# Optimization experiments

Measured on AMD Instinct MI355X. Metric: run time of the kernel, lower is better.

## Reference

```python
import jax, jax.numpy as jnp
import numpy as np

B, N, M, D, OUT, K = 8, 32, 64, 128, 128, 3
EPS = 1e-5


def batchnorm(x, g, b):
    # training-mode BatchNorm2d over NCHW (stats over B,H,W per channel, biased var)
    mean = x.mean((0, 2, 3), keepdims=True)
    var = ((x - mean) ** 2).mean((0, 2, 3), keepdims=True)
    return g[None, :, None, None] * (x - mean) * jax.lax.rsqrt(var + EPS) + b[None, :, None, None]


def mycorr(x):
    # Pearson correlation between nodes along feature dim: x (B,M,N,D) -> (B,M,N,N)
    xc = x - x.mean(-1, keepdims=True)
    num = jnp.einsum('bmid,bmjd->bmij', xc, xc)
    nrm = jnp.sqrt((xc * xc).sum(-1))
    return num / (nrm[:, :, :, None] * nrm[:, :, None, :] + 1e-8)


def attention(x, W_fc1, W_fc2):
    # x: (B,M,N,D). AdaptiveAvgPool2d((None,1)) over the concat [Wh_i, pos*Wh_j]
    # equals 0.5*(mean_d Wh_i + mean_d(pos*Wh_j)); pos=1 where Wh_i==Wh_j else 2.
    adj = mycorr(x)
    mean_i = x.mean(-1)                       # (B,M,N)
    xi = x[:, :, :, None, :]                  # (B,M,N,1,D)
    xj = x[:, :, None, :, :]                  # (B,M,1,N,D)
    alt_mean = jnp.where(xi == xj, xj, 2.0 * xj).mean(-1)  # (B,M,N,N)
    e = 0.5 * (mean_i[:, :, :, None] + alt_mean)            # (B,M,N,N)
    ef = e.reshape(e.shape[0], e.shape[1], -1)              # (B,M,N*N) pair channels
    h = jax.nn.relu(jnp.einsum('rp,bmp->bmr', W_fc1, ef))
    e2 = jax.nn.sigmoid(jnp.einsum('pr,bmr->bmp', W_fc2, h)).reshape(e.shape)
    att = jax.nn.softmax(jnp.where(adj > 0, e2, jnp.float32(-1e12)), axis=-1)
    return jnp.einsum('bmij,bmjd->bmid', att, x)


def setup_inputs() -> dict:
    key = jax.random.key(0)
    ks = jax.random.split(key, 8)
    P, r, s = N * N, (N * N) // 2, 0.05
    return {
        'x': jax.random.normal(ks[0], (B, N, M, D), jnp.float32),
        'W_sc': jax.random.normal(ks[1], (OUT, M), jnp.float32) * s,
        'g_sc': jnp.ones(OUT, jnp.float32), 'b_sc': jnp.zeros(OUT, jnp.float32),
        'W_l1': jax.random.normal(ks[2], (M, M), jnp.float32) * s,
        'g1': jnp.ones(M, jnp.float32), 'b1': jnp.zeros(M, jnp.float32),
        'W_fc1': jax.random.normal(ks[3], (r, P), jnp.float32) * s,
        'W_fc2': jax.random.normal(ks[4], (P, r), jnp.float32) * s,
        'g2': jnp.ones(M, jnp.float32), 'b2': jnp.zeros(M, jnp.float32),
        'W_dw': jax.random.normal(ks[5], (N, 1, K, K), jnp.float32) * s,
        'g3': jnp.ones(N, jnp.float32), 'b3': jnp.zeros(N, jnp.float32),
        'W_l3': jax.random.normal(ks[6], (OUT, M), jnp.float32) * s,
    }


def reference(x, W_sc, g_sc, b_sc, W_l1, g1, b1, W_fc1, W_fc2, g2, b2, W_dw, g3, b3, W_l3):
    xm = jnp.transpose(x, (0, 2, 1, 3))  # (B,M,N,D)
    # shortcut: 1x1 conv over head channel + BN (stride=1 path)
    shortcut = batchnorm(jnp.einsum('om,bmnd->bond', W_sc, xm), g_sc, b_sc)
    # layer_1: 1x1 conv, BN, global node attention, BN, ReLU
    out = batchnorm(jnp.einsum('cm,bmnd->bcnd', W_l1, xm), g1, b1)
    out = attention(out, W_fc1, W_fc2)
    out = jax.nn.relu(batchnorm(out, g2, b2))
    # layer_2: depthwise KxK conv over (head, dim) per node, BN, ReLU
    out = jnp.transpose(out, (0, 2, 1, 3))  # (B,N,M,D)
    pad = K // 2
    out = jax.lax.conv_general_dilated(out, W_dw, (1, 1), ((pad, pad), (pad, pad)),
                                       feature_group_count=N,
                                       dimension_numbers=('NCHW', 'OIHW', 'NCHW'))
    out = jax.nn.relu(batchnorm(out, g3, b3))
    # layer_3: 1x1 conv to out_channels heads + residual
    out = jnp.transpose(out, (0, 2, 1, 3))  # (B,M,N,D)
    out = jnp.einsum('om,bmnd->bond', W_l3, out) + shortcut
    return jnp.transpose(out, (0, 2, 1, 3))  # (B,N,OUT,D)
```

## Files before the change

kernel.cpp:

```cpp
#include <hip/hip_runtime.h>
#include <math.h>

#define EPS 1e-5f


__device__ __forceinline__ void fma4(float4& a, float s, const float4& v) {
    a.x += s * v.x; a.y += s * v.y; a.z += s * v.z; a.w += s * v.w;
}

__global__ __launch_bounds__(256) void k1_matmul_stats(
    const float* __restrict__ x, const float* __restrict__ Wsc,
    const float* __restrict__ Wl1, float* __restrict__ t_sc,
    float* __restrict__ t_l1, float* __restrict__ stats)
{
    int g  = blockIdx.x;
    int bn = blockIdx.y;
    int b = bn >> 5, n = bn & 31;
    __shared__ __align__(16) float s_x[64 * 128];
    __shared__ __align__(16) float s_wT[64 * 68];
    int t = threadIdx.x;

    const float4* xg = (const float4*)(x + (size_t)bn * 8192);
    for (int i = t; i < 2048; i += 256) ((float4*)s_x)[i] = xg[i];

    const float* wbase = (g < 2) ? (Wsc + (size_t)g * 64 * 64) : Wl1;
    for (int i = t; i < 1024; i += 256) {
        int m = i >> 4, rq = (i & 15) * 4;
        float4 wv;
        wv.x = wbase[(size_t)(rq + 0) * 64 + m];
        wv.y = wbase[(size_t)(rq + 1) * 64 + m];
        wv.z = wbase[(size_t)(rq + 2) * 64 + m];
        wv.w = wbase[(size_t)(rq + 3) * 64 + m];
        *(float4*)(s_wT + m * 68 + rq) = wv;
    }
    __syncthreads();

    int wv = t >> 6, lane = t & 63;
    int dl = lane & 15;
    int g4 = lane >> 4;
    int d0 = dl * 8;
    int c0 = wv * 16 + g4 * 4;

    float4 acc[4][2];
#pragma unroll
    for (int i = 0; i < 4; i++) { acc[i][0] = make_float4(0,0,0,0); acc[i][1] = make_float4(0,0,0,0); }

    for (int m = 0; m < 64; m += 2) {
        float4 x00 = *(const float4*)(s_x + m * 128 + d0);
        float4 x01 = *(const float4*)(s_x + m * 128 + d0 + 4);
        float4 x10 = *(const float4*)(s_x + (m + 1) * 128 + d0);
        float4 x11 = *(const float4*)(s_x + (m + 1) * 128 + d0 + 4);
        float4 w0 = *(const float4*)(s_wT + m * 68 + c0);
        float4 w1 = *(const float4*)(s_wT + (m + 1) * 68 + c0);
        fma4(acc[0][0], w0.x, x00); fma4(acc[0][1], w0.x, x01);
        fma4(acc[1][0], w0.y, x00); fma4(acc[1][1], w0.y, x01);
        fma4(acc[2][0], w0.z, x00); fma4(acc[2][1], w0.z, x01);
        fma4(acc[3][0], w0.w, x00); fma4(acc[3][1], w0.w, x01);
        fma4(acc[0][0], w1.x, x10); fma4(acc[0][1], w1.x, x11);
        fma4(acc[1][0], w1.y, x10); fma4(acc[1][1], w1.y, x11);
        fma4(acc[2][0], w1.z, x10); fma4(acc[2][1], w1.z, x11);
        fma4(acc[3][0], w1.w, x10); fma4(acc[3][1], w1.w, x11);
    }

#pragma unroll
    for (int i = 0; i < 4; i++) {
        int cc = g * 64 + c0 + i;
        float4 v0 = acc[i][0], v1 = acc[i][1];
        float* dst;
        if (cc < 128) dst = t_sc + (((size_t)(b * 128 + cc)) * 32 + n) * 128 + d0;
        else          dst = t_l1 + (((size_t)(b * 64 + (cc - 128))) * 32 + n) * 128 + d0;
        *(float4*)dst = v0;
        *(float4*)(dst + 4) = v1;
        float s = v0.x + v0.y + v0.z + v0.w + v1.x + v1.y + v1.z + v1.w;
        float q = v0.x*v0.x + v0.y*v0.y + v0.z*v0.z + v0.w*v0.w
                + v1.x*v1.x + v1.y*v1.y + v1.z*v1.z + v1.w*v1.w;
#pragma unroll
        for (int off = 8; off > 0; off >>= 1) {
            s += __shfl_down(s, off, 16);
            q += __shfl_down(q, off, 16);
        }
        if (dl == 0) {
            if (cc < 128) {
                atomicAdd(&stats[cc], s);
                atomicAdd(&stats[cc + 128], q);
            } else {
                atomicAdd(&stats[256 + (cc - 128)], s);
                atomicAdd(&stats[320 + (cc - 128)], q);
            }
        }
    }
}

__global__ __launch_bounds__(256) void k2_attn_prep(
    const float* __restrict__ t_l1, const float* __restrict__ g1,
    const float* __restrict__ b1, const float* __restrict__ stats,
    float* __restrict__ y_g, float* __restrict__ E,
    unsigned int* __restrict__ maskbits)
{
    int bm = blockIdx.x;
    int t  = threadIdx.x;
    __shared__ __align__(16) float y_s[32 * 132];
    __shared__ float S_s[32];
    __shared__ unsigned int m_s[32];
    int m = bm & 63;
    float mean = stats[256 + m] * (1.0f / 32768.0f);
    float var  = stats[320 + m] * (1.0f / 32768.0f) - mean * mean;
    float a = g1[m] * rsqrtf(var + EPS);
    float c = b1[m] - a * mean;

    if (t < 32) m_s[t] = 0u;
    const float4* src = (const float4*)(t_l1 + (size_t)bm * 4096);
    for (int i = t; i < 1024; i += 256) {
        float4 v = src[i];
        v.x = a * v.x + c; v.y = a * v.y + c; v.z = a * v.z + c; v.w = a * v.w + c;
        int row = i >> 5, col = (i & 31) * 4;
        *(float4*)(y_s + row * 132 + col) = v;
    }
    __syncthreads();

    {
        int r = t >> 3, j = t & 7;
        float s = 0.f;
        const float* yr = y_s + r * 132 + j * 16;
#pragma unroll
        for (int dd = 0; dd < 16; dd++) s += yr[dd];
#pragma unroll
        for (int off = 4; off > 0; off >>= 1) s += __shfl_down(s, off, 8);
        if (j == 0) S_s[r] = s;
    }
    __syncthreads();

    int i = t >> 3, j0 = (t & 7) * 4;
    float dot[4] = {0.f, 0.f, 0.f, 0.f};
    float eqs[4] = {0.f, 0.f, 0.f, 0.f};
    const float* yi = y_s + i * 132;
    for (int dq = 0; dq < 32; dq++) {
        float4 a4 = *(const float4*)(yi + dq * 4);
#pragma unroll
        for (int q = 0; q < 4; q++) {
            float4 b4 = *(const float4*)(y_s + (j0 + q) * 132 + dq * 4);
            dot[q] += a4.x * b4.x + a4.y * b4.y + a4.z * b4.z + a4.w * b4.w;
            eqs[q] += (a4.x == b4.x ? b4.x : 0.f) + (a4.y == b4.y ? b4.y : 0.f)
                    + (a4.z == b4.z ? b4.z : 0.f) + (a4.w == b4.w ? b4.w : 0.f);
        }
    }
    float Si = S_s[i];
    unsigned int bits = 0u;
    float ev[4];
#pragma unroll
    for (int q = 0; q < 4; q++) {
        float Sj = S_s[j0 + q];
        float num = dot[q] - Si * Sj * (1.0f / 128.0f);
        if (num > 0.f) bits |= (1u << (j0 + q));
        ev[q] = (Si + 2.f * Sj - eqs[q]) * (1.0f / 256.0f);
    }
    atomicOr(&m_s[i], bits);
    *(float4*)(E + (size_t)bm * 1024 + i * 32 + j0) = make_float4(ev[0], ev[1], ev[2], ev[3]);
    __syncthreads();
    if (t < 32) maskbits[bm * 32 + t] = m_s[t];

    float4* yd = (float4*)(y_g + (size_t)bm * 4096);
    for (int idx = t; idx < 1024; idx += 256) {
        int row = idx >> 5, col = (idx & 31) * 4;
        yd[idx] = *(const float4*)(y_s + row * 132 + col);
    }
}

template<int KDIM, int MODE>
__global__ __launch_bounds__(256) void k3_gemm(
    const float* __restrict__ A, const float* __restrict__ Bm,
    float* __restrict__ C, int NC)
{
    __shared__ __align__(16) float lds[4 * 2304];
    int t = threadIdx.x;
    int w = t >> 6, l = t & 63;
    int ct = blockIdx.x, rt = blockIdx.y;
    int row0 = rt * 32, col0 = ct * 32;
    float* As = lds + w * 2304;
    float* Bs = As + 1152;
    int rg = l >> 3;
    int cg = l & 7;
    int kq = (l & 7) * 4;
    constexpr int SLABS = KDIM / 128;

    float4 acc[4];
#pragma unroll
    for (int ii = 0; ii < 4; ii++) acc[ii] = make_float4(0,0,0,0);

    float4 av[4], bv[4], av2[4], bv2[4];
    int k0 = w * 32;
#pragma unroll
    for (int rr = 0; rr < 4; rr++) {
        int r = rg + rr * 8;
        av[rr] = *(const float4*)(A  + (size_t)(row0 + r) * KDIM + k0 + kq);
        bv[rr] = *(const float4*)(Bm + (size_t)(col0 + r) * KDIM + k0 + kq);
    }

    for (int s = 0; s < SLABS; s++) {
#pragma unroll
        for (int rr = 0; rr < 4; rr++) {
            int r = rg + rr * 8;
            As[(kq + 0) * 36 + r] = av[rr].x; As[(kq + 1) * 36 + r] = av[rr].y;
            As[(kq + 2) * 36 + r] = av[rr].z; As[(kq + 3) * 36 + r] = av[rr].w;
            Bs[(kq + 0) * 36 + r] = bv[rr].x; Bs[(kq + 1) * 36 + r] = bv[rr].y;
            Bs[(kq + 2) * 36 + r] = bv[rr].z; Bs[(kq + 3) * 36 + r] = bv[rr].w;
        }
        if (s + 1 < SLABS) {
            int kn = (4 * (s + 1) + w) * 32;
#pragma unroll
            for (int rr = 0; rr < 4; rr++) {
                int r = rg + rr * 8;
                av2[rr] = *(const float4*)(A  + (size_t)(row0 + r) * KDIM + kn + kq);
                bv2[rr] = *(const float4*)(Bm + (size_t)(col0 + r) * KDIM + kn + kq);
            }
        }
#pragma unroll
        for (int k = 0; k < 32; k++) {
            float4 a = *(const float4*)(As + k * 36 + rg * 4);
            float4 b = *(const float4*)(Bs + k * 36 + cg * 4);
            fma4(acc[0], a.x, b);
            fma4(acc[1], a.y, b);
            fma4(acc[2], a.z, b);
            fma4(acc[3], a.w, b);
        }
#pragma unroll
        for (int rr = 0; rr < 4; rr++) { av[rr] = av2[rr]; bv[rr] = bv2[rr]; }
    }

    __syncthreads();
    float* red = lds;
#pragma unroll
    for (int ii = 0; ii < 4; ii++)
        *(float4*)(red + w * 1024 + (rg * 4 + ii) * 32 + cg * 4) = acc[ii];
    __syncthreads();

    int r = t >> 3, c4 = (t & 7) * 4;
    float4 s0 = *(const float4*)(red + r * 32 + c4);
    float4 s1 = *(const float4*)(red + 1024 + r * 32 + c4);
    float4 s2 = *(const float4*)(red + 2048 + r * 32 + c4);
    float4 s3 = *(const float4*)(red + 3072 + r * 32 + c4);
    float4 v;
    v.x = s0.x + s1.x + s2.x + s3.x;
    v.y = s0.y + s1.y + s2.y + s3.y;
    v.z = s0.z + s1.z + s2.z + s3.z;
    v.w = s0.w + s1.w + s2.w + s3.w;
    if (MODE == 0) {
        v.x = fmaxf(v.x, 0.f); v.y = fmaxf(v.y, 0.f);
        v.z = fmaxf(v.z, 0.f); v.w = fmaxf(v.w, 0.f);
    } else {
        v.x = 1.0f / (1.0f + expf(-v.x)); v.y = 1.0f / (1.0f + expf(-v.y));
        v.z = 1.0f / (1.0f + expf(-v.z)); v.w = 1.0f / (1.0f + expf(-v.w));
    }
    *(float4*)(C + (size_t)(row0 + r) * NC + col0 + c4) = v;
}

__global__ __launch_bounds__(256) void k4_attn_apply(
    const float* __restrict__ E2, const unsigned int* __restrict__ maskbits,
    const float* __restrict__ y_g, float* __restrict__ att_out,
    float* __restrict__ stats)
{
    int bm = blockIdx.x;
    int t  = threadIdx.x;
    __shared__ __align__(16) float att_s[32 * 33];
    __shared__ __align__(16) float y_sh[32 * 128];
    __shared__ float redS[4], redQ[4];

    const float4* ysrc = (const float4*)(y_g + (size_t)bm * 4096);
    float4* yds = (float4*)y_sh;
    for (int i = t; i < 1024; i += 256) yds[i] = ysrc[i];

    {
        int r = t >> 3, j0 = (t & 7) * 4;
        unsigned int mk = maskbits[bm * 32 + r];
        float4 e4 = *(const float4*)(E2 + (size_t)bm * 1024 + r * 32 + j0);
        float v0 = ((mk >> (j0 + 0)) & 1u) ? e4.x : -1e12f;
        float v1 = ((mk >> (j0 + 1)) & 1u) ? e4.y : -1e12f;
        float v2 = ((mk >> (j0 + 2)) & 1u) ? e4.z : -1e12f;
        float v3 = ((mk >> (j0 + 3)) & 1u) ? e4.w : -1e12f;
        float mx = fmaxf(fmaxf(v0, v1), fmaxf(v2, v3));
#pragma unroll
        for (int off = 1; off < 8; off <<= 1) mx = fmaxf(mx, __shfl_xor(mx, off, 8));
        float e0 = __expf(v0 - mx), e1 = __expf(v1 - mx);
        float e2 = __expf(v2 - mx), e3 = __expf(v3 - mx);
        float s = e0 + e1 + e2 + e3;
#pragma unroll
        for (int off = 1; off < 8; off <<= 1) s += __shfl_xor(s, off, 8);
        float inv = 1.0f / s;
        att_s[r * 33 + j0 + 0] = e0 * inv;
        att_s[r * 33 + j0 + 1] = e1 * inv;
        att_s[r * 33 + j0 + 2] = e2 * inv;
        att_s[r * 33 + j0 + 3] = e3 * inv;
    }
    __syncthreads();

    int tx = t & 31, ty = t >> 5;
    int dq = tx * 4;
    float ssum = 0.f, sq = 0.f;
#pragma unroll
    for (int ii = 0; ii < 4; ii++) {
        int i = ty * 4 + ii;
        float4 acc = make_float4(0.f, 0.f, 0.f, 0.f);
        for (int j = 0; j < 32; j++) {
            float aw = att_s[i * 33 + j];
            float4 yv = *(const float4*)(y_sh + j * 128 + dq);
            acc.x += aw * yv.x; acc.y += aw * yv.y;
            acc.z += aw * yv.z; acc.w += aw * yv.w;
        }
        *(float4*)(att_out + (size_t)bm * 4096 + i * 128 + dq) = acc;
        ssum += acc.x + acc.y + acc.z + acc.w;
        sq   += acc.x * acc.x + acc.y * acc.y + acc.z * acc.z + acc.w * acc.w;
    }
#pragma unroll
    for (int off = 32; off > 0; off >>= 1) {
        ssum += __shfl_down(ssum, off, 64);
        sq   += __shfl_down(sq, off, 64);
    }
    int wave = t >> 6, lane = t & 63;
    if (lane == 0) { redS[wave] = ssum; redQ[wave] = sq; }
    __syncthreads();
    if (t == 0) {
        float S = redS[0] + redS[1] + redS[2] + redS[3];
        float Q = redQ[0] + redQ[1] + redQ[2] + redQ[3];
        int m = bm & 63;
        atomicAdd(&stats[384 + m], S);
        atomicAdd(&stats[448 + m], Q);
    }
}

__global__ __launch_bounds__(256) void k5_conv(
    const float* __restrict__ att_out, const float* __restrict__ Wdw,
    const float* __restrict__ g2, const float* __restrict__ b2,
    float* __restrict__ stats, float* __restrict__ v_g)
{
    int bn = blockIdx.x;
    int b = bn >> 5, n = bn & 31;
    int t = threadIdx.x;
    __shared__ __align__(16) float z_s[66 * 130];
    __shared__ float a2_s[64], c2_s[64];
    __shared__ float redS[4], redQ[4];

    if (t < 64) {
        float mean = stats[384 + t] * (1.0f / 32768.0f);
        float var  = stats[448 + t] * (1.0f / 32768.0f) - mean * mean;
        float a = g2[t] * rsqrtf(var + EPS);
        a2_s[t] = a; c2_s[t] = b2[t] - a * mean;
    }
    for (int i = t; i < 66 * 130; i += 256) z_s[i] = 0.f;
    __syncthreads();

    for (int i = t; i < 2048; i += 256) {
        int m = i >> 5, c4 = (i & 31) * 4;
        float4 vv = *(const float4*)(att_out + (((size_t)(b * 64 + m)) * 32 + n) * 128 + c4);
        float a = a2_s[m], c = c2_s[m];
        float* dst = z_s + (m + 1) * 130 + c4 + 1;
        dst[0] = fmaxf(a * vv.x + c, 0.f);
        dst[1] = fmaxf(a * vv.y + c, 0.f);
        dst[2] = fmaxf(a * vv.z + c, 0.f);
        dst[3] = fmaxf(a * vv.w + c, 0.f);
    }
    float w[9];
#pragma unroll
    for (int i = 0; i < 9; i++) w[i] = Wdw[n * 9 + i];
    __syncthreads();

    int tx = t & 31, ty = t >> 5;
    int d0 = tx * 4;
    float ssum = 0.f, sq = 0.f;
#pragma unroll
    for (int rr = 0; rr < 8; rr++) {
        int h = ty * 8 + rr;
        float o0 = 0.f, o1 = 0.f, o2 = 0.f, o3 = 0.f;
#pragma unroll
        for (int dh = 0; dh < 3; dh++) {
            const float* zr = z_s + (h + dh) * 130 + d0;
#pragma unroll
            for (int dw = 0; dw < 3; dw++) {
                float wv = w[dh * 3 + dw];
                o0 += wv * zr[dw + 0];
                o1 += wv * zr[dw + 1];
                o2 += wv * zr[dw + 2];
                o3 += wv * zr[dw + 3];
            }
        }
        *(float4*)(v_g + ((size_t)bn * 64 + h) * 128 + d0) = make_float4(o0, o1, o2, o3);
        ssum += o0 + o1 + o2 + o3;
        sq   += o0 * o0 + o1 * o1 + o2 * o2 + o3 * o3;
    }
#pragma unroll
    for (int off = 32; off > 0; off >>= 1) {
        ssum += __shfl_down(ssum, off, 64);
        sq   += __shfl_down(sq, off, 64);
    }
    int wave = t >> 6, lane = t & 63;
    if (lane == 0) { redS[wave] = ssum; redQ[wave] = sq; }
    __syncthreads();
    if (t == 0) {
        atomicAdd(&stats[512 + n], redS[0] + redS[1] + redS[2] + redS[3]);
        atomicAdd(&stats[544 + n], redQ[0] + redQ[1] + redQ[2] + redQ[3]);
    }
}

__global__ __launch_bounds__(256) void k6_final(
    const float* __restrict__ v_g, const float* __restrict__ t_sc,
    const float* __restrict__ Wl3, const float* __restrict__ g3,
    const float* __restrict__ b3, const float* __restrict__ gsc,
    const float* __restrict__ bsc, const float* __restrict__ stats,
    float* __restrict__ outp)
{
    int oh = blockIdx.x;
    int bn = blockIdx.y;
    int b = bn >> 5, n = bn & 31;
    int t = threadIdx.x;
    __shared__ __align__(16) float z_s[64 * 128];
    __shared__ __align__(16) float s_wT[64 * 68];

    float mean3 = stats[512 + n] * (1.0f / 65536.0f);
    float var3  = stats[544 + n] * (1.0f / 65536.0f) - mean3 * mean3;
    float a3 = g3[n] * rsqrtf(var3 + EPS);
    float c3 = b3[n] - a3 * mean3;

    const float4* vsrc = (const float4*)(v_g + (size_t)bn * 8192);
    for (int i = t; i < 2048; i += 256) {
        float4 vv = vsrc[i];
        float4 r;
        r.x = fmaxf(a3 * vv.x + c3, 0.f);
        r.y = fmaxf(a3 * vv.y + c3, 0.f);
        r.z = fmaxf(a3 * vv.z + c3, 0.f);
        r.w = fmaxf(a3 * vv.w + c3, 0.f);
        ((float4*)z_s)[i] = r;
    }
    const float* wbase = Wl3 + (size_t)oh * 64 * 64;
    for (int i = t; i < 1024; i += 256) {
        int m = i >> 4, rq = (i & 15) * 4;
        float4 wv;
        wv.x = wbase[(size_t)(rq + 0) * 64 + m];
        wv.y = wbase[(size_t)(rq + 1) * 64 + m];
        wv.z = wbase[(size_t)(rq + 2) * 64 + m];
        wv.w = wbase[(size_t)(rq + 3) * 64 + m];
        *(float4*)(s_wT + m * 68 + rq) = wv;
    }
    __syncthreads();

    int wv = t >> 6, lane = t & 63;
    int dl = lane & 15, g4 = lane >> 4;
    int d0 = dl * 8;
    int c0 = wv * 16 + g4 * 4;

    float4 acc[4][2];
#pragma unroll
    for (int i = 0; i < 4; i++) { acc[i][0] = make_float4(0,0,0,0); acc[i][1] = make_float4(0,0,0,0); }

    for (int m = 0; m < 64; m += 2) {
        float4 x00 = *(const float4*)(z_s + m * 128 + d0);
        float4 x01 = *(const float4*)(z_s + m * 128 + d0 + 4);
        float4 x10 = *(const float4*)(z_s + (m + 1) * 128 + d0);
        float4 x11 = *(const float4*)(z_s + (m + 1) * 128 + d0 + 4);
        float4 w0 = *(const float4*)(s_wT + m * 68 + c0);
        float4 w1 = *(const float4*)(s_wT + (m + 1) * 68 + c0);
        fma4(acc[0][0], w0.x, x00); fma4(acc[0][1], w0.x, x01);
        fma4(acc[1][0], w0.y, x00); fma4(acc[1][1], w0.y, x01);
        fma4(acc[2][0], w0.z, x00); fma4(acc[2][1], w0.z, x01);
        fma4(acc[3][0], w0.w, x00); fma4(acc[3][1], w0.w, x01);
        fma4(acc[0][0], w1.x, x10); fma4(acc[0][1], w1.x, x11);
        fma4(acc[1][0], w1.y, x10); fma4(acc[1][1], w1.y, x11);
        fma4(acc[2][0], w1.z, x10); fma4(acc[2][1], w1.z, x11);
        fma4(acc[3][0], w1.w, x10); fma4(acc[3][1], w1.w, x11);
    }

#pragma unroll
    for (int i = 0; i < 4; i++) {
        int o = oh * 64 + c0 + i;
        float msc = stats[o] * (1.0f / 32768.0f);
        float vsc = stats[128 + o] * (1.0f / 32768.0f) - msc * msc;
        float asc = gsc[o] * rsqrtf(vsc + EPS);
        float csc = bsc[o] - asc * msc;
        const float* ts = t_sc + (((size_t)(b * 128 + o)) * 32 + n) * 128 + d0;
        float4 t0 = *(const float4*)(ts);
        float4 t1 = *(const float4*)(ts + 4);
        float4 o0 = acc[i][0], o1 = acc[i][1];
        o0.x += asc * t0.x + csc; o0.y += asc * t0.y + csc;
        o0.z += asc * t0.z + csc; o0.w += asc * t0.w + csc;
        o1.x += asc * t1.x + csc; o1.y += asc * t1.y + csc;
        o1.z += asc * t1.z + csc; o1.w += asc * t1.w + csc;
        float* dst = outp + (((size_t)(b * 32 + n)) * 128 + o) * 128 + d0;
        *(float4*)dst = o0;
        *(float4*)(dst + 4) = o1;
    }
}

extern "C" void kernel_launch(void* const* d_in, const int* in_sizes, int n_in,
                              void* d_out, int out_size, void* d_ws, size_t ws_size,
                              hipStream_t stream)
{
    const float* x    = (const float*)d_in[0];
    const float* Wsc  = (const float*)d_in[1];
    const float* gsc  = (const float*)d_in[2];
    const float* bsc  = (const float*)d_in[3];
    const float* Wl1  = (const float*)d_in[4];
    const float* g1   = (const float*)d_in[5];
    const float* b1   = (const float*)d_in[6];
    const float* Wfc1 = (const float*)d_in[7];
    const float* Wfc2 = (const float*)d_in[8];
    const float* g2   = (const float*)d_in[9];
    const float* b2   = (const float*)d_in[10];
    const float* Wdw  = (const float*)d_in[11];
    const float* g3   = (const float*)d_in[12];
    const float* b3   = (const float*)d_in[13];
    const float* Wl3  = (const float*)d_in[14];
    float* outp = (float*)d_out;

    float* ws = (float*)d_ws;
    float* stats = ws;
    float* t_sc  = ws + 1024;
    float* t_l1  = t_sc + 4194304;
    float* y_g   = t_l1 + 2097152;
    float* E     = y_g + 2097152;
    float* H     = E + 524288;
    float* E2    = H + 262144;
    unsigned int* maskb = (unsigned int*)(E2 + 524288);

    (void)hipMemsetAsync(stats, 0, 1024 * sizeof(float), stream);

    k1_matmul_stats<<<dim3(3, 256), 256, 0, stream>>>(x, Wsc, Wl1, t_sc, t_l1, stats);
    k2_attn_prep<<<512, 256, 0, stream>>>(t_l1, g1, b1, stats, y_g, E, maskb);
    k3_gemm<1024, 0><<<dim3(16, 16), 256, 0, stream>>>(E, Wfc1, H, 512);
    k3_gemm<512, 1><<<dim3(32, 16), 256, 0, stream>>>(H, Wfc2, E2, 1024);
    k4_attn_apply<<<512, 256, 0, stream>>>(E2, maskb, y_g, t_l1, stats);
    k5_conv<<<256, 256, 0, stream>>>(t_l1, Wdw, g2, b2, stats, y_g);
    k6_final<<<dim3(2, 256), 256, 0, stream>>>(y_g, t_sc, Wl3, g3, b3, gsc, bsc, stats, outp);
}
```

Measured before the change: 210.5 us.

## Fuse all stages into one persistent cooperative kernel with grid syncs

Turns the seven stage kernels into device functions that share one union of shared memory, and runs them from a single persistent cooperative kernel. Stages are separated by grid-wide barriers, and each block loops over work units. The aim is to remove launch overhead and the gaps between kernels. In exchange, every block reserves the largest shared-memory footprint, the grid is capped at 256 or 512 blocks so each stage runs in fewer waves, and grid.sync adds cost; the separate-launch path remains as a fallback if the cooperative launch fails.

```diff
diff --git a/kernel.cpp b/kernel.cpp
--- a/kernel.cpp
+++ b/kernel.cpp
@@ -1,5 +1,8 @@
 #include <hip/hip_runtime.h>
+#include <hip/hip_cooperative_groups.h>
 #include <math.h>
+
+namespace cg = cooperative_groups;
 
 #define EPS 1e-5f
 
@@ -8,17 +11,23 @@
     a.x += s * v.x; a.y += s * v.y; a.z += s * v.z; a.w += s * v.w;
 }
 
-__global__ __launch_bounds__(256) void k1_matmul_stats(
-    const float* __restrict__ x, const float* __restrict__ Wsc,
+union SharedU {
+    struct { float s_x[64 * 128]; float s_wT[64 * 68]; } p1;
+    struct { float y_s[32 * 132]; float S_s[32]; unsigned int m_s[32]; } p2;
+    struct { float lds[4 * 2304]; } p3;
+    struct { float att_s[32 * 33]; float y_sh[32 * 128]; float redS[4], redQ[4]; } p5;
+    struct { float z_s[66 * 130]; float a2_s[64], c2_s[64]; float redS[4], redQ[4]; } p6;
+    struct { float z_s[64 * 128]; float s_wT[64 * 68]; } p7;
+};
+
+__device__ __forceinline__ void phase1(
+    SharedU& su, const float* __restrict__ x, const float* __restrict__ Wsc,
     const float* __restrict__ Wl1, float* __restrict__ t_sc,
-    float* __restrict__ t_l1, float* __restrict__ stats)
-{
-    int g  = blockIdx.x;
-    int bn = blockIdx.y;
+    float* __restrict__ t_l1, float* __restrict__ stats, int g, int bn, int t)
+{
+    float* s_x  = su.p1.s_x;
+    float* s_wT = su.p1.s_wT;
     int b = bn >> 5, n = bn & 31;
-    __shared__ __align__(16) float s_x[64 * 128];
-    __shared__ __align__(16) float s_wT[64 * 68];
-    int t = threadIdx.x;
 
     const float4* xg = (const float4*)(x + (size_t)bn * 8192);
     for (int i = t; i < 2048; i += 256) ((float4*)s_x)[i] = xg[i];
@@ -91,17 +100,15 @@
     }
 }
 
-__global__ __launch_bounds__(256) void k2_attn_prep(
-    const float* __restrict__ t_l1, const float* __restrict__ g1,
+__device__ __forceinline__ void phase2(
+    SharedU& su, const float* __restrict__ t_l1, const float* __restrict__ g1,
     const float* __restrict__ b1, const float* __restrict__ stats,
     float* __restrict__ y_g, float* __restrict__ E,
-    unsigned int* __restrict__ maskbits)
-{
-    int bm = blockIdx.x;
-    int t  = threadIdx.x;
-    __shared__ __align__(16) float y_s[32 * 132];
-    __shared__ float S_s[32];
-    __shared__ unsigned int m_s[32];
+    unsigned int* __restrict__ maskbits, int bm, int t)
+{
+    float* y_s = su.p2.y_s;
+    float* S_s = su.p2.S_s;
+    unsigned int* m_s = su.p2.m_s;
     int m = bm & 63;
     float mean = stats[256 + m] * (1.0f / 32768.0f);
     float var  = stats[320 + m] * (1.0f / 32768.0f) - mean * mean;
@@ -167,14 +174,12 @@
 }
 
 template<int KDIM, int MODE>
-__global__ __launch_bounds__(256) void k3_gemm(
-    const float* __restrict__ A, const float* __restrict__ Bm,
-    float* __restrict__ C, int NC)
-{
-    __shared__ __align__(16) float lds[4 * 2304];
-    int t = threadIdx.x;
+__device__ __forceinline__ void gemm_phase(
+    SharedU& su, const float* __restrict__ A, const float* __restrict__ Bm,
+    float* __restrict__ C, int NC, int ct, int rt, int t)
+{
+    float* lds = su.p3.lds;
     int w = t >> 6, l = t & 63;
-    int ct = blockIdx.x, rt = blockIdx.y;
     int row0 = rt * 32, col0 = ct * 32;
     float* As = lds + w * 2304;
     float* Bs = As + 1152;
@@ -254,16 +259,15 @@
     *(float4*)(C + (size_t)(row0 + r) * NC + col0 + c4) = v;
 }
 
-__global__ __launch_bounds__(256) void k4_attn_apply(
-    const float* __restrict__ E2, const unsigned int* __restrict__ maskbits,
-    const float* __restrict__ y_g, float* __restrict__ att_out,
-    float* __restrict__ stats)
-{
-    int bm = blockIdx.x;
-    int t  = threadIdx.x;
-    __shared__ __align__(16) float att_s[32 * 33];
-    __shared__ __align__(16) float y_sh[32 * 128];
-    __shared__ float redS[4], redQ[4];
+__device__ __forceinline__ void phase5(
+    SharedU& su, const float* __restrict__ E2,
+    const unsigned int* __restrict__ maskbits, const float* __restrict__ y_g,
+    float* __restrict__ att_out, float* __restrict__ stats, int bm, int t)
+{
+    float* att_s = su.p5.att_s;
+    float* y_sh  = su.p5.y_sh;
+    float* redS  = su.p5.redS;
+    float* redQ  = su.p5.redQ;
 
     const float4* ysrc = (const float4*)(y_g + (size_t)bm * 4096);
     float4* yds = (float4*)y_sh;
@@ -327,17 +331,17 @@
     }
 }
 
-__global__ __launch_bounds__(256) void k5_conv(
-    const float* __restrict__ att_out, const float* __restrict__ Wdw,
+__device__ __forceinline__ void phase6(
+    SharedU& su, const float* __restrict__ att_out, const float* __restrict__ Wdw,
     const float* __restrict__ g2, const float* __restrict__ b2,
-    float* __restrict__ stats, float* __restrict__ v_g)
-{
-    int bn = blockIdx.x;
+    float* __restrict__ stats, float* __restrict__ v_g, int bn, int t)
+{
+    float* z_s = su.p6.z_s;
+    float* a2_s = su.p6.a2_s;
+    float* c2_s = su.p6.c2_s;
+    float* redS = su.p6.redS;
+    float* redQ = su.p6.redQ;
     int b = bn >> 5, n = bn & 31;
-    int t = threadIdx.x;
-    __shared__ __align__(16) float z_s[66 * 130];
-    __shared__ float a2_s[64], c2_s[64];
-    __shared__ float redS[4], redQ[4];
 
     if (t < 64) {
         float mean = stats[384 + t] * (1.0f / 32768.0f);
@@ -400,19 +404,16 @@
     }
 }
 
-__global__ __launch_bounds__(256) void k6_final(
-    const float* __restrict__ v_g, const float* __restrict__ t_sc,
+__device__ __forceinline__ void phase7(
+    SharedU& su, const float* __restrict__ v_g, const float* __restrict__ t_sc,
     const float* __restrict__ Wl3, const float* __restrict__ g3,
     const float* __restrict__ b3, const float* __restrict__ gsc,
     const float* __restrict__ bsc, const float* __restrict__ stats,
-    float* __restrict__ outp)
-{
-    int oh = blockIdx.x;
-    int bn = blockIdx.y;
+    float* __restrict__ outp, int oh, int bn, int t)
+{
+    float* z_s  = su.p7.z_s;
+    float* s_wT = su.p7.s_wT;
     int b = bn >> 5, n = bn & 31;
-    int t = threadIdx.x;
-    __shared__ __align__(16) float z_s[64 * 128];
-    __shared__ __align__(16) float s_wT[64 * 68];
 
     float mean3 = stats[512 + n] * (1.0f / 65536.0f);
     float var3  = stats[544 + n] * (1.0f / 65536.0f) - mean3 * mean3;
@@ -488,6 +489,115 @@
     }
 }
 
+__global__ __launch_bounds__(256, 2) void mega(
+    const float* x, const float* Wsc, const float* gsc, const float* bsc,
+    const float* Wl1, const float* g1, const float* b1,
+    const float* Wfc1, const float* Wfc2, const float* g2, const float* b2,
+    const float* Wdw, const float* g3, const float* b3, const float* Wl3,
+    float* stats, float* t_sc, float* t_l1, float* y_g,
+    float* E, float* H, float* E2, unsigned int* maskb, float* outp)
+{
+    __shared__ SharedU su;
+    cg::grid_group grid = cg::this_grid();
+    int blk = blockIdx.x;
+    int t = threadIdx.x;
+    int gsz = gridDim.x;
+
+    for (int u = blk; u < 768; u += gsz) {
+        phase1(su, x, Wsc, Wl1, t_sc, t_l1, stats, u >> 8, u & 255, t);
+        __syncthreads();
+    }
+    grid.sync();
+
+    for (int u = blk; u < 512; u += gsz) {
+        phase2(su, t_l1, g1, b1, stats, y_g, E, maskb, u, t);
+        __syncthreads();
+    }
+    grid.sync();
+
+    for (int u = blk; u < 256; u += gsz) {
+        gemm_phase<1024, 0>(su, E, Wfc1, H, 512, u & 15, u >> 4, t);
+        __syncthreads();
+    }
+    grid.sync();
+
+    for (int u = blk; u < 512; u += gsz) {
+        gemm_phase<512, 1>(su, H, Wfc2, E2, 1024, u & 31, u >> 5, t);
+        __syncthreads();
+    }
+    grid.sync();
+
+    for (int u = blk; u < 512; u += gsz) {
+        phase5(su, E2, maskb, y_g, t_l1, stats, u, t);
+        __syncthreads();
+    }
+    grid.sync();
+
+    for (int u = blk; u < 256; u += gsz) {
+        phase6(su, t_l1, Wdw, g2, b2, stats, y_g, u, t);
+        __syncthreads();
+    }
+    grid.sync();
+
+    for (int u = blk; u < 512; u += gsz) {
+        phase7(su, y_g, t_sc, Wl3, g3, b3, gsc, bsc, stats, outp, u & 1, u >> 1, t);
+        __syncthreads();
+    }
+}
+
+__global__ __launch_bounds__(256) void k1_w(
+    const float* __restrict__ x, const float* __restrict__ Wsc,
+    const float* __restrict__ Wl1, float* __restrict__ t_sc,
+    float* __restrict__ t_l1, float* __restrict__ stats)
+{
+    __shared__ SharedU su;
+    phase1(su, x, Wsc, Wl1, t_sc, t_l1, stats, blockIdx.x, blockIdx.y, threadIdx.x);
+}
+__global__ __launch_bounds__(256) void k2_w(
+    const float* __restrict__ t_l1, const float* __restrict__ g1,
+    const float* __restrict__ b1, const float* __restrict__ stats,
+    float* __restrict__ y_g, float* __restrict__ E,
+    unsigned int* __restrict__ maskbits)
+{
+    __shared__ SharedU su;
+    phase2(su, t_l1, g1, b1, stats, y_g, E, maskbits, blockIdx.x, threadIdx.x);
+}
+template<int KDIM, int MODE>
+__global__ __launch_bounds__(256) void k3_w(
+    const float* __restrict__ A, const float* __restrict__ Bm,
+    float* __restrict__ C, int NC)
+{
+    __shared__ SharedU su;
+    gemm_phase<KDIM, MODE>(su, A, Bm, C, NC, blockIdx.x, blockIdx.y, threadIdx.x);
+}
+__global__ __launch_bounds__(256) void k5_w(
+    const float* __restrict__ E2, const unsigned int* __restrict__ maskbits,
+    const float* __restrict__ y_g, float* __restrict__ att_out,
+    float* __restrict__ stats)
+{
+    __shared__ SharedU su;
+    phase5(su, E2, maskbits, y_g, att_out, stats, blockIdx.x, threadIdx.x);
+}
+__global__ __launch_bounds__(256) void k6_w(
+    const float* __restrict__ att_out, const float* __restrict__ Wdw,
+    const float* __restrict__ g2, const float* __restrict__ b2,
+    float* __restrict__ stats, float* __restrict__ v_g)
+{
+    __shared__ SharedU su;
+    phase6(su, att_out, Wdw, g2, b2, stats, v_g, blockIdx.x, threadIdx.x);
+}
+__global__ __launch_bounds__(256) void k7_w(
+    const float* __restrict__ v_g, const float* __restrict__ t_sc,
+    const float* __restrict__ Wl3, const float* __restrict__ g3,
+    const float* __restrict__ b3, const float* __restrict__ gsc,
+    const float* __restrict__ bsc, const float* __restrict__ stats,
+    float* __restrict__ outp)
+{
+    __shared__ SharedU su;
+    phase7(su, v_g, t_sc, Wl3, g3, b3, gsc, bsc, stats, outp,
+           blockIdx.x, blockIdx.y, threadIdx.x);
+}
+
 extern "C" void kernel_launch(void* const* d_in, const int* in_sizes, int n_in,
                               void* d_out, int out_size, void* d_ws, size_t ws_size,
                               hipStream_t stream)
@@ -521,11 +631,26 @@
 
     (void)hipMemsetAsync(stats, 0, 1024 * sizeof(float), stream);
 
-    k1_matmul_stats<<<dim3(3, 256), 256, 0, stream>>>(x, Wsc, Wl1, t_sc, t_l1, stats);
-    k2_attn_prep<<<512, 256, 0, stream>>>(t_l1, g1, b1, stats, y_g, E, maskb);
-    k3_gemm<1024, 0><<<dim3(16, 16), 256, 0, stream>>>(E, Wfc1, H, 512);
-    k3_gemm<512, 1><<<dim3(32, 16), 256, 0, stream>>>(H, Wfc2, E2, 1024);
-    k4_attn_apply<<<512, 256, 0, stream>>>(E2, maskb, y_g, t_l1, stats);
-    k5_conv<<<256, 256, 0, stream>>>(t_l1, Wdw, g2, b2, stats, y_g);
-    k6_final<<<dim3(2, 256), 256, 0, stream>>>(y_g, t_sc, Wl3, g3, b3, gsc, bsc, stats, outp);
-}
+    int perCU = 0;
+    hipError_t qerr = hipOccupancyMaxActiveBlocksPerMultiprocessor(&perCU, mega, 256, 0);
+    int nblk = (qerr == hipSuccess && perCU >= 2) ? 512 : 256;
+
+    void* args[] = {
+        (void*)&x, (void*)&Wsc, (void*)&gsc, (void*)&bsc, (void*)&Wl1,
+        (void*)&g1, (void*)&b1, (void*)&Wfc1, (void*)&Wfc2, (void*)&g2,
+        (void*)&b2, (void*)&Wdw, (void*)&g3, (void*)&b3, (void*)&Wl3,
+        (void*)&stats, (void*)&t_sc, (void*)&t_l1, (void*)&y_g,
+        (void*)&E, (void*)&H, (void*)&E2, (void*)&maskb, (void*)&outp
+    };
+    hipError_t lerr = hipLaunchCooperativeKernel((void*)mega, dim3(nblk), dim3(256),
+                                                 args, 0, stream);
+    if (lerr != hipSuccess) {
+        k1_w<<<dim3(3, 256), 256, 0, stream>>>(x, Wsc, Wl1, t_sc, t_l1, stats);
+        k2_w<<<512, 256, 0, stream>>>(t_l1, g1, b1, stats, y_g, E, maskb);
+        k3_w<1024, 0><<<dim3(16, 16), 256, 0, stream>>>(E, Wfc1, H, 512);
+        k3_w<512, 1><<<dim3(32, 16), 256, 0, stream>>>(H, Wfc2, E2, 1024);
+        k5_w<<<512, 256, 0, stream>>>(E2, maskb, y_g, t_l1, stats);
+        k6_w<<<256, 256, 0, stream>>>(t_l1, Wdw, g2, b2, stats, y_g);
+        k7_w<<<dim3(2, 256), 256, 0, stream>>>(y_g, t_sc, Wl3, g3, b3, gsc, bsc, stats, outp);
+    }
+}
```

New measurement: 443.9 us. 111% more time.

## Split-K the attention FC GEMMs and double grid sizes of attention/conv kernels

Applied to the files above, without the earlier changes.

The two FC GEMMs now use split-K with two partial outputs, and the following kernels sum the partials and apply ReLU or sigmoid. This replaces the templated GEMM with activation epilogues. The attention-prep, attention-apply and depthwise conv kernels are each split in half (row halves or D halves, with halo loading for the conv), doubling block counts so more CUs stay busy. The cost is extra partial-buffer traffic and some redundant loads of shared inputs per half-block.

```diff
diff --git a/kernel.cpp b/kernel.cpp
--- a/kernel.cpp
+++ b/kernel.cpp
@@ -8,7 +8,7 @@
     a.x += s * v.x; a.y += s * v.y; a.z += s * v.z; a.w += s * v.w;
 }
 
-__global__ __launch_bounds__(256) void k1_matmul_stats(
+__global__ __launch_bounds__(256) void k1_w(
     const float* __restrict__ x, const float* __restrict__ Wsc,
     const float* __restrict__ Wl1, float* __restrict__ t_sc,
     float* __restrict__ t_l1, float* __restrict__ stats)
@@ -36,8 +36,7 @@
     __syncthreads();
 
     int wv = t >> 6, lane = t & 63;
-    int dl = lane & 15;
-    int g4 = lane >> 4;
+    int dl = lane & 15, g4 = lane >> 4;
     int d0 = dl * 8;
     int c0 = wv * 16 + g4 * 4;
 
@@ -91,30 +90,30 @@
     }
 }
 
-__global__ __launch_bounds__(256) void k2_attn_prep(
+__global__ __launch_bounds__(256) void k2_w(
     const float* __restrict__ t_l1, const float* __restrict__ g1,
     const float* __restrict__ b1, const float* __restrict__ stats,
     float* __restrict__ y_g, float* __restrict__ E,
     unsigned int* __restrict__ maskbits)
 {
-    int bm = blockIdx.x;
+    int blk = blockIdx.x;
+    int bm = blk >> 1, h = blk & 1;
     int t  = threadIdx.x;
     __shared__ __align__(16) float y_s[32 * 132];
     __shared__ float S_s[32];
-    __shared__ unsigned int m_s[32];
+    __shared__ unsigned int m_s[16];
     int m = bm & 63;
     float mean = stats[256 + m] * (1.0f / 32768.0f);
     float var  = stats[320 + m] * (1.0f / 32768.0f) - mean * mean;
     float a = g1[m] * rsqrtf(var + EPS);
     float c = b1[m] - a * mean;
 
-    if (t < 32) m_s[t] = 0u;
+    if (t < 16) m_s[t] = 0u;
     const float4* src = (const float4*)(t_l1 + (size_t)bm * 4096);
     for (int i = t; i < 1024; i += 256) {
         float4 v = src[i];
         v.x = a * v.x + c; v.y = a * v.y + c; v.z = a * v.z + c; v.w = a * v.w + c;
-        int row = i >> 5, col = (i & 31) * 4;
-        *(float4*)(y_s + row * 132 + col) = v;
+        *(float4*)(y_s + (i >> 5) * 132 + (i & 31) * 4) = v;
     }
     __syncthreads();
 
@@ -130,58 +129,61 @@
     }
     __syncthreads();
 
-    int i = t >> 3, j0 = (t & 7) * 4;
-    float dot[4] = {0.f, 0.f, 0.f, 0.f};
-    float eqs[4] = {0.f, 0.f, 0.f, 0.f};
-    const float* yi = y_s + i * 132;
+    int i_loc = t >> 4;
+    int i = h * 16 + i_loc;
+    int j0 = (t & 15) * 2;
+    float dot0 = 0.f, dot1 = 0.f, eq0 = 0.f, eq1 = 0.f;
+    const float* yi  = y_s + i * 132;
+    const float* yj0 = y_s + j0 * 132;
+    const float* yj1 = y_s + (j0 + 1) * 132;
     for (int dq = 0; dq < 32; dq++) {
         float4 a4 = *(const float4*)(yi + dq * 4);
-#pragma unroll
-        for (int q = 0; q < 4; q++) {
-            float4 b4 = *(const float4*)(y_s + (j0 + q) * 132 + dq * 4);
-            dot[q] += a4.x * b4.x + a4.y * b4.y + a4.z * b4.z + a4.w * b4.w;
-            eqs[q] += (a4.x == b4.x ? b4.x : 0.f) + (a4.y == b4.y ? b4.y : 0.f)
-                    + (a4.z == b4.z ? b4.z : 0.f) + (a4.w == b4.w ? b4.w : 0.f);
-        }
+        float4 b0 = *(const float4*)(yj0 + dq * 4);
+        float4 b1v = *(const float4*)(yj1 + dq * 4);
+        dot0 += a4.x * b0.x + a4.y * b0.y + a4.z * b0.z + a4.w * b0.w;
+        eq0  += (a4.x == b0.x ? b0.x : 0.f) + (a4.y == b0.y ? b0.y : 0.f)
+              + (a4.z == b0.z ? b0.z : 0.f) + (a4.w == b0.w ? b0.w : 0.f);
+        dot1 += a4.x * b1v.x + a4.y * b1v.y + a4.z * b1v.z + a4.w * b1v.w;
+        eq1  += (a4.x == b1v.x ? b1v.x : 0.f) + (a4.y == b1v.y ? b1v.y : 0.f)
+              + (a4.z == b1v.z ? b1v.z : 0.f) + (a4.w == b1v.w ? b1v.w : 0.f);
     }
     float Si = S_s[i];
+    float Sj0 = S_s[j0], Sj1 = S_s[j0 + 1];
     unsigned int bits = 0u;
-    float ev[4];
-#pragma unroll
-    for (int q = 0; q < 4; q++) {
-        float Sj = S_s[j0 + q];
-        float num = dot[q] - Si * Sj * (1.0f / 128.0f);
-        if (num > 0.f) bits |= (1u << (j0 + q));
-        ev[q] = (Si + 2.f * Sj - eqs[q]) * (1.0f / 256.0f);
-    }
-    atomicOr(&m_s[i], bits);
-    *(float4*)(E + (size_t)bm * 1024 + i * 32 + j0) = make_float4(ev[0], ev[1], ev[2], ev[3]);
-    __syncthreads();
-    if (t < 32) maskbits[bm * 32 + t] = m_s[t];
+    if (dot0 - Si * Sj0 * (1.0f / 128.0f) > 0.f) bits |= (1u << j0);
+    if (dot1 - Si * Sj1 * (1.0f / 128.0f) > 0.f) bits |= (1u << (j0 + 1));
+    float ev0 = (Si + 2.f * Sj0 - eq0) * (1.0f / 256.0f);
+    float ev1 = (Si + 2.f * Sj1 - eq1) * (1.0f / 256.0f);
+    atomicOr(&m_s[i_loc], bits);
+    *(float2*)(E + (size_t)bm * 1024 + i * 32 + j0) = make_float2(ev0, ev1);
+    __syncthreads();
+    if (t < 16) maskbits[bm * 32 + h * 16 + t] = m_s[t];
 
     float4* yd = (float4*)(y_g + (size_t)bm * 4096);
-    for (int idx = t; idx < 1024; idx += 256) {
-        int row = idx >> 5, col = (idx & 31) * 4;
-        yd[idx] = *(const float4*)(y_s + row * 132 + col);
-    }
-}
-
-template<int KDIM, int MODE>
-__global__ __launch_bounds__(256) void k3_gemm(
+    for (int idx = t; idx < 512; idx += 256) {
+        int row = h * 16 + (idx >> 5), col = (idx & 31) * 4;
+        yd[h * 512 + idx] = *(const float4*)(y_s + row * 132 + col);
+    }
+}
+
+__global__ __launch_bounds__(256) void k3a_w(
     const float* __restrict__ A, const float* __restrict__ Bm,
-    float* __restrict__ C, int NC)
+    float* __restrict__ Cp)
 {
     __shared__ __align__(16) float lds[4 * 2304];
+    int blk = blockIdx.x;
+    int kz = blk >> 8, tile = blk & 255;
+    int ct = tile & 15, rt = tile >> 4;
+    const float* Ab = A + kz * 512;
+    const float* Bb = Bm + kz * 512;
+    float* C = Cp + (size_t)kz * 262144;
     int t = threadIdx.x;
     int w = t >> 6, l = t & 63;
-    int ct = blockIdx.x, rt = blockIdx.y;
     int row0 = rt * 32, col0 = ct * 32;
     float* As = lds + w * 2304;
     float* Bs = As + 1152;
-    int rg = l >> 3;
-    int cg = l & 7;
-    int kq = (l & 7) * 4;
-    constexpr int SLABS = KDIM / 128;
+    int rg = l >> 3, cg = l & 7, kq = (l & 7) * 4;
+    const int SLABS = 4, KROW = 1024;
 
     float4 acc[4];
 #pragma unroll
@@ -192,10 +194,9 @@
 #pragma unroll
     for (int rr = 0; rr < 4; rr++) {
         int r = rg + rr * 8;
-        av[rr] = *(const float4*)(A  + (size_t)(row0 + r) * KDIM + k0 + kq);
-        bv[rr] = *(const float4*)(Bm + (size_t)(col0 + r) * KDIM + k0 + kq);
-    }
-
+        av[rr] = *(const float4*)(Ab + (size_t)(row0 + r) * KROW + k0 + kq);
+        bv[rr] = *(const float4*)(Bb + (size_t)(col0 + r) * KROW + k0 + kq);
+    }
     for (int s = 0; s < SLABS; s++) {
 #pragma unroll
         for (int rr = 0; rr < 4; rr++) {
@@ -210,18 +211,16 @@
 #pragma unroll
             for (int rr = 0; rr < 4; rr++) {
                 int r = rg + rr * 8;
-                av2[rr] = *(const float4*)(A  + (size_t)(row0 + r) * KDIM + kn + kq);
-                bv2[rr] = *(const float4*)(Bm + (size_t)(col0 + r) * KDIM + kn + kq);
+                av2[rr] = *(const float4*)(Ab + (size_t)(row0 + r) * KROW + kn + kq);
+                bv2[rr] = *(const float4*)(Bb + (size_t)(col0 + r) * KROW + kn + kq);
             }
         }
 #pragma unroll
         for (int k = 0; k < 32; k++) {
             float4 a = *(const float4*)(As + k * 36 + rg * 4);
             float4 b = *(const float4*)(Bs + k * 36 + cg * 4);
-            fma4(acc[0], a.x, b);
-            fma4(acc[1], a.y, b);
-            fma4(acc[2], a.z, b);
-            fma4(acc[3], a.w, b);
+            fma4(acc[0], a.x, b); fma4(acc[1], a.y, b);
+            fma4(acc[2], a.z, b); fma4(acc[3], a.w, b);
         }
 #pragma unroll
         for (int rr = 0; rr < 4; rr++) { av[rr] = av2[rr]; bv[rr] = bv2[rr]; }
@@ -244,52 +243,136 @@
     v.y = s0.y + s1.y + s2.y + s3.y;
     v.z = s0.z + s1.z + s2.z + s3.z;
     v.w = s0.w + s1.w + s2.w + s3.w;
-    if (MODE == 0) {
-        v.x = fmaxf(v.x, 0.f); v.y = fmaxf(v.y, 0.f);
-        v.z = fmaxf(v.z, 0.f); v.w = fmaxf(v.w, 0.f);
-    } else {
-        v.x = 1.0f / (1.0f + expf(-v.x)); v.y = 1.0f / (1.0f + expf(-v.y));
-        v.z = 1.0f / (1.0f + expf(-v.z)); v.w = 1.0f / (1.0f + expf(-v.w));
-    }
-    *(float4*)(C + (size_t)(row0 + r) * NC + col0 + c4) = v;
-}
-
-__global__ __launch_bounds__(256) void k4_attn_apply(
-    const float* __restrict__ E2, const unsigned int* __restrict__ maskbits,
-    const float* __restrict__ y_g, float* __restrict__ att_out,
-    float* __restrict__ stats)
-{
-    int bm = blockIdx.x;
+    *(float4*)(C + (size_t)(row0 + r) * 512 + col0 + c4) = v;
+}
+
+__global__ __launch_bounds__(256) void k4a_w(
+    const float* __restrict__ H0, const float* __restrict__ H1,
+    const float* __restrict__ Bm, float* __restrict__ Cp)
+{
+    __shared__ __align__(16) float lds[4 * 2304];
+    int blk = blockIdx.x;
+    int kz = blk >> 9, tile = blk & 511;
+    int ct = tile & 31, rt = tile >> 5;
+    const float* H0b = H0 + kz * 256;
+    const float* H1b = H1 + kz * 256;
+    const float* Bb  = Bm + kz * 256;
+    float* C = Cp + (size_t)kz * 524288;
+    int t = threadIdx.x;
+    int w = t >> 6, l = t & 63;
+    int row0 = rt * 32, col0 = ct * 32;
+    float* As = lds + w * 2304;
+    float* Bs = As + 1152;
+    int rg = l >> 3, cg = l & 7, kq = (l & 7) * 4;
+    const int SLABS = 2, KROW = 512;
+
+    float4 acc[4];
+#pragma unroll
+    for (int ii = 0; ii < 4; ii++) acc[ii] = make_float4(0,0,0,0);
+
+    float4 av[4], bv[4], av2[4], bv2[4];
+    int k0 = w * 32;
+#pragma unroll
+    for (int rr = 0; rr < 4; rr++) {
+        int r = rg + rr * 8;
+        size_t ai = (size_t)(row0 + r) * KROW + k0 + kq;
+        float4 h0 = *(const float4*)(H0b + ai);
+        float4 h1 = *(const float4*)(H1b + ai);
+        av[rr].x = fmaxf(h0.x + h1.x, 0.f); av[rr].y = fmaxf(h0.y + h1.y, 0.f);
+        av[rr].z = fmaxf(h0.z + h1.z, 0.f); av[rr].w = fmaxf(h0.w + h1.w, 0.f);
+        bv[rr] = *(const float4*)(Bb + (size_t)(col0 + r) * KROW + k0 + kq);
+    }
+    for (int s = 0; s < SLABS; s++) {
+#pragma unroll
+        for (int rr = 0; rr < 4; rr++) {
+            int r = rg + rr * 8;
+            As[(kq + 0) * 36 + r] = av[rr].x; As[(kq + 1) * 36 + r] = av[rr].y;
+            As[(kq + 2) * 36 + r] = av[rr].z; As[(kq + 3) * 36 + r] = av[rr].w;
+            Bs[(kq + 0) * 36 + r] = bv[rr].x; Bs[(kq + 1) * 36 + r] = bv[rr].y;
+            Bs[(kq + 2) * 36 + r] = bv[rr].z; Bs[(kq + 3) * 36 + r] = bv[rr].w;
+        }
+        if (s + 1 < SLABS) {
+            int kn = (4 * (s + 1) + w) * 32;
+#pragma unroll
+            for (int rr = 0; rr < 4; rr++) {
+                int r = rg + rr * 8;
+                size_t ai = (size_t)(row0 + r) * KROW + kn + kq;
+                float4 h0 = *(const float4*)(H0b + ai);
+                float4 h1 = *(const float4*)(H1b + ai);
+                av2[rr].x = fmaxf(h0.x + h1.x, 0.f); av2[rr].y = fmaxf(h0.y + h1.y, 0.f);
+                av2[rr].z = fmaxf(h0.z + h1.z, 0.f); av2[rr].w = fmaxf(h0.w + h1.w, 0.f);
+                bv2[rr] = *(const float4*)(Bb + (size_t)(col0 + r) * KROW + kn + kq);
+            }
+        }
+#pragma unroll
+        for (int k = 0; k < 32; k++) {
+            float4 a = *(const float4*)(As + k * 36 + rg * 4);
+            float4 b = *(const float4*)(Bs + k * 36 + cg * 4);
+            fma4(acc[0], a.x, b); fma4(acc[1], a.y, b);
+            fma4(acc[2], a.z, b); fma4(acc[3], a.w, b);
+        }
+#pragma unroll
+        for (int rr = 0; rr < 4; rr++) { av[rr] = av2[rr]; bv[rr] = bv2[rr]; }
+    }
+
+    __syncthreads();
+    float* red = lds;
+#pragma unroll
+    for (int ii = 0; ii < 4; ii++)
+        *(float4*)(red + w * 1024 + (rg * 4 + ii) * 32 + cg * 4) = acc[ii];
+    __syncthreads();
+
+    int r = t >> 3, c4 = (t & 7) * 4;
+    float4 s0 = *(const float4*)(red + r * 32 + c4);
+    float4 s1 = *(const float4*)(red + 1024 + r * 32 + c4);
+    float4 s2 = *(const float4*)(red + 2048 + r * 32 + c4);
+    float4 s3 = *(const float4*)(red + 3072 + r * 32 + c4);
+    float4 v;
+    v.x = s0.x + s1.x + s2.x + s3.x;
+    v.y = s0.y + s1.y + s2.y + s3.y;
+    v.z = s0.z + s1.z + s2.z + s3.z;
+    v.w = s0.w + s1.w + s2.w + s3.w;
+    *(float4*)(C + (size_t)(row0 + r) * 1024 + col0 + c4) = v;
+}
+
+__global__ __launch_bounds__(256) void k5_w(
+    const float* __restrict__ E2a, const float* __restrict__ E2b,
+    const unsigned int* __restrict__ maskbits, const float* __restrict__ y_g,
+    float* __restrict__ att_out, float* __restrict__ stats)
+{
+    int blk = blockIdx.x;
+    int bm = blk >> 1, h = blk & 1;
     int t  = threadIdx.x;
-    __shared__ __align__(16) float att_s[32 * 33];
+    __shared__ __align__(16) float att_s[16 * 33];
     __shared__ __align__(16) float y_sh[32 * 128];
     __shared__ float redS[4], redQ[4];
 
     const float4* ysrc = (const float4*)(y_g + (size_t)bm * 4096);
-    float4* yds = (float4*)y_sh;
-    for (int i = t; i < 1024; i += 256) yds[i] = ysrc[i];
+    for (int i = t; i < 1024; i += 256) ((float4*)y_sh)[i] = ysrc[i];
 
     {
-        int r = t >> 3, j0 = (t & 7) * 4;
+        int r_loc = t >> 4;
+        int r = h * 16 + r_loc;
+        int j0 = (t & 15) * 2;
         unsigned int mk = maskbits[bm * 32 + r];
-        float4 e4 = *(const float4*)(E2 + (size_t)bm * 1024 + r * 32 + j0);
-        float v0 = ((mk >> (j0 + 0)) & 1u) ? e4.x : -1e12f;
-        float v1 = ((mk >> (j0 + 1)) & 1u) ? e4.y : -1e12f;
-        float v2 = ((mk >> (j0 + 2)) & 1u) ? e4.z : -1e12f;
-        float v3 = ((mk >> (j0 + 3)) & 1u) ? e4.w : -1e12f;
-        float mx = fmaxf(fmaxf(v0, v1), fmaxf(v2, v3));
-#pragma unroll
-        for (int off = 1; off < 8; off <<= 1) mx = fmaxf(mx, __shfl_xor(mx, off, 8));
-        float e0 = __expf(v0 - mx), e1 = __expf(v1 - mx);
-        float e2 = __expf(v2 - mx), e3 = __expf(v3 - mx);
-        float s = e0 + e1 + e2 + e3;
-#pragma unroll
-        for (int off = 1; off < 8; off <<= 1) s += __shfl_xor(s, off, 8);
-        float inv = 1.0f / s;
-        att_s[r * 33 + j0 + 0] = e0 * inv;
-        att_s[r * 33 + j0 + 1] = e1 * inv;
-        att_s[r * 33 + j0 + 2] = e2 * inv;
-        att_s[r * 33 + j0 + 3] = e3 * inv;
+        size_t eidx = (size_t)bm * 1024 + r * 32 + j0;
+        float2 ea = *(const float2*)(E2a + eidx);
+        float2 eb = *(const float2*)(E2b + eidx);
+        float s0r = ea.x + eb.x, s1r = ea.y + eb.y;
+        float e0 = 1.0f / (1.0f + expf(-s0r));
+        float e1 = 1.0f / (1.0f + expf(-s1r));
+        float v0 = ((mk >> (j0 + 0)) & 1u) ? e0 : -1e12f;
+        float v1 = ((mk >> (j0 + 1)) & 1u) ? e1 : -1e12f;
+        float mx = fmaxf(v0, v1);
+#pragma unroll
+        for (int off = 1; off < 16; off <<= 1) mx = fmaxf(mx, __shfl_xor(mx, off, 16));
+        float x0 = __expf(v0 - mx), x1 = __expf(v1 - mx);
+        float sm = x0 + x1;
+#pragma unroll
+        for (int off = 1; off < 16; off <<= 1) sm += __shfl_xor(sm, off, 16);
+        float inv = 1.0f / sm;
+        att_s[r_loc * 33 + j0 + 0] = x0 * inv;
+        att_s[r_loc * 33 + j0 + 1] = x1 * inv;
     }
     __syncthreads();
 
@@ -297,11 +380,12 @@
     int dq = tx * 4;
     float ssum = 0.f, sq = 0.f;
 #pragma unroll
-    for (int ii = 0; ii < 4; ii++) {
-        int i = ty * 4 + ii;
+    for (int ii = 0; ii < 2; ii++) {
+        int i_loc = ty * 2 + ii;
+        int i = h * 16 + i_loc;
         float4 acc = make_float4(0.f, 0.f, 0.f, 0.f);
         for (int j = 0; j < 32; j++) {
-            float aw = att_s[i * 33 + j];
+            float aw = att_s[i_loc * 33 + j];
             float4 yv = *(const float4*)(y_sh + j * 128 + dq);
             acc.x += aw * yv.x; acc.y += aw * yv.y;
             acc.z += aw * yv.z; acc.w += aw * yv.w;
@@ -327,15 +411,17 @@
     }
 }
 
-__global__ __launch_bounds__(256) void k5_conv(
+__global__ __launch_bounds__(256) void k6_w(
     const float* __restrict__ att_out, const float* __restrict__ Wdw,
     const float* __restrict__ g2, const float* __restrict__ b2,
     float* __restrict__ stats, float* __restrict__ v_g)
 {
-    int bn = blockIdx.x;
+    int blk = blockIdx.x;
+    int bn = blk >> 1, h = blk & 1;
     int b = bn >> 5, n = bn & 31;
+    int dbase = h * 64;
     int t = threadIdx.x;
-    __shared__ __align__(16) float z_s[66 * 130];
+    __shared__ float z_s[66 * 68];
     __shared__ float a2_s[64], c2_s[64];
     __shared__ float redS[4], redQ[4];
 
@@ -345,34 +431,42 @@
         float a = g2[t] * rsqrtf(var + EPS);
         a2_s[t] = a; c2_s[t] = b2[t] - a * mean;
     }
-    for (int i = t; i < 66 * 130; i += 256) z_s[i] = 0.f;
-    __syncthreads();
-
-    for (int i = t; i < 2048; i += 256) {
-        int m = i >> 5, c4 = (i & 31) * 4;
-        float4 vv = *(const float4*)(att_out + (((size_t)(b * 64 + m)) * 32 + n) * 128 + c4);
+    for (int i = t; i < 66 * 68; i += 256) z_s[i] = 0.f;
+    __syncthreads();
+
+    for (int i = t; i < 1024; i += 256) {
+        int m = i >> 4, c4 = (i & 15) * 4;
+        float4 vv = *(const float4*)(att_out + (((size_t)(b * 64 + m)) * 32 + n) * 128 + dbase + c4);
         float a = a2_s[m], c = c2_s[m];
-        float* dst = z_s + (m + 1) * 130 + c4 + 1;
+        float* dst = z_s + (m + 1) * 68 + 1 + c4;
         dst[0] = fmaxf(a * vv.x + c, 0.f);
         dst[1] = fmaxf(a * vv.y + c, 0.f);
         dst[2] = fmaxf(a * vv.z + c, 0.f);
         dst[3] = fmaxf(a * vv.w + c, 0.f);
     }
+    if (t < 128) {
+        int m = t & 63, side = t >> 6;
+        int d = dbase + (side ? 64 : -1);
+        if (d >= 0 && d < 128) {
+            float val = att_out[(((size_t)(b * 64 + m)) * 32 + n) * 128 + d];
+            z_s[(m + 1) * 68 + (side ? 65 : 0)] = fmaxf(a2_s[m] * val + c2_s[m], 0.f);
+        }
+    }
     float w[9];
 #pragma unroll
     for (int i = 0; i < 9; i++) w[i] = Wdw[n * 9 + i];
     __syncthreads();
 
-    int tx = t & 31, ty = t >> 5;
+    int tx = t & 15, ty = t >> 4;
     int d0 = tx * 4;
     float ssum = 0.f, sq = 0.f;
 #pragma unroll
-    for (int rr = 0; rr < 8; rr++) {
-        int h = ty * 8 + rr;
+    for (int rr = 0; rr < 4; rr++) {
+        int hr = ty * 4 + rr;
         float o0 = 0.f, o1 = 0.f, o2 = 0.f, o3 = 0.f;
 #pragma unroll
         for (int dh = 0; dh < 3; dh++) {
-            const float* zr = z_s + (h + dh) * 130 + d0;
+            const float* zr = z_s + (hr + dh) * 68 + d0;
 #pragma unroll
             for (int dw = 0; dw < 3; dw++) {
                 float wv = w[dh * 3 + dw];
@@ -382,7 +476,7 @@
                 o3 += wv * zr[dw + 3];
             }
         }
-        *(float4*)(v_g + ((size_t)bn * 64 + h) * 128 + d0) = make_float4(o0, o1, o2, o3);
+        *(float4*)(v_g + ((size_t)bn * 64 + hr) * 128 + dbase + d0) = make_float4(o0, o1, o2, o3);
         ssum += o0 + o1 + o2 + o3;
         sq   += o0 * o0 + o1 * o1 + o2 * o2 + o3 * o3;
     }
@@ -400,7 +494,7 @@
     }
 }
 
-__global__ __launch_bounds__(256) void k6_final(
+__global__ __launch_bounds__(256) void k7_w(
     const float* __restrict__ v_g, const float* __restrict__ t_sc,
     const float* __restrict__ Wl3, const float* __restrict__ g3,
     const float* __restrict__ b3, const float* __restrict__ gsc,
@@ -515,17 +609,19 @@
     float* t_l1  = t_sc + 4194304;
     float* y_g   = t_l1 + 2097152;
     float* E     = y_g + 2097152;
-    float* H     = E + 524288;
-    float* E2    = H + 262144;
-    unsigned int* maskb = (unsigned int*)(E2 + 524288);
+    float* H0    = E + 524288;
+    float* H1    = H0 + 262144;
+    float* E2a   = H1 + 262144;
+    float* E2b   = E2a + 524288;
+    unsigned int* maskb = (unsigned int*)(E2b + 524288);
 
     (void)hipMemsetAsync(stats, 0, 1024 * sizeof(float), stream);
 
-    k1_matmul_stats<<<dim3(3, 256), 256, 0, stream>>>(x, Wsc, Wl1, t_sc, t_l1, stats);
-    k2_attn_prep<<<512, 256, 0, stream>>>(t_l1, g1, b1, stats, y_g, E, maskb);
-    k3_gemm<1024, 0><<<dim3(16, 16), 256, 0, stream>>>(E, Wfc1, H, 512);
-    k3_gemm<512, 1><<<dim3(32, 16), 256, 0, stream>>>(H, Wfc2, E2, 1024);
-    k4_attn_apply<<<512, 256, 0, stream>>>(E2, maskb, y_g, t_l1, stats);
-    k5_conv<<<256, 256, 0, stream>>>(t_l1, Wdw, g2, b2, stats, y_g);
-    k6_final<<<dim3(2, 256), 256, 0, stream>>>(y_g, t_sc, Wl3, g3, b3, gsc, bsc, stats, outp);
-}
+    k1_w<<<dim3(3, 256), 256, 0, stream>>>(x, Wsc, Wl1, t_sc, t_l1, stats);
+    k2_w<<<1024, 256, 0, stream>>>(t_l1, g1, b1, stats, y_g, E, maskb);
+    k3a_w<<<512, 256, 0, stream>>>(E, Wfc1, H0);
+    k4a_w<<<1024, 256, 0, stream>>>(H0, H1, Wfc2, E2a);
+    k5_w<<<1024, 256, 0, stream>>>(E2a, E2b, maskb, y_g, t_l1, stats);
+    k6_w<<<512, 256, 0, stream>>>(t_l1, Wdw, g2, b2, stats, y_g);
+    k7_w<<<dim3(2, 256), 256, 0, stream>>>(y_g, t_sc, Wl3, g3, b3, gsc, bsc, stats, outp);
+}
```

New measurement: 213.8 us. About the same (+1.6%).
